# Performance work log

Measured on AMD Instinct MI355X. Metric: run time of the kernel, lower is better.

The kernel has to match this reference:

```python
import jax, jax.numpy as jnp
import numpy as np

N_VARS = 8192
N_CHECKS = 4096
DC = 6          # check degree (edges per check)
DV = 3          # variable degree
N_EDGES = N_CHECKS * DC  # == N_VARS * DV == 24576
NUM_ITERS = 5
BATCH = 2048


def setup_inputs() -> dict:
    key = jax.random.key(0)
    k1, _ = jax.random.split(key)
    channel_llrs = jax.random.normal(k1, (BATCH, N_VARS), dtype=jnp.float32)
    # Regular Tanner graph: edges sorted by check (constant degree DC),
    # variable side is a random permutation with each var appearing DV times.
    H_rows = jnp.asarray(np.repeat(np.arange(N_CHECKS), DC), dtype=jnp.int32)
    rng = np.random.default_rng(0)
    H_cols = jnp.asarray(rng.permutation(np.repeat(np.arange(N_VARS), DV)), dtype=jnp.int32)
    weights = jnp.full((NUM_ITERS, 1), 0.5, dtype=jnp.float32)  # nn.Parameter init
    return {"channel_llrs": channel_llrs, "weights": weights,
            "H_rows": H_rows, "H_cols": H_cols, "n_checks": N_CHECKS}


def _decode(channel_llrs, weights, H_cols, n_checks):
    B, n_vars = channel_llrs.shape
    E = H_cols.shape[0]
    dc = E // n_checks  # constant check degree (edges sorted by check)
    pos = jnp.arange(dc)
    c2v = jnp.zeros((B, E), dtype=channel_llrs.dtype)
    for i in range(weights.shape[0]):
        # variable-node update: sum incoming c2v per variable, exclude self edge
        agg = jnp.zeros((B, n_vars), dtype=channel_llrs.dtype).at[:, H_cols].add(c2v)
        var_llrs = channel_llrs + agg
        v2c = var_llrs[:, H_cols] - c2v                      # [B, E]
        # check-node update (min-sum with self-exclusion), grouped per check
        g = v2c.reshape(B, n_checks, dc)                     # [B, C, dc]
        s = jnp.sign(g)
        prod_s = jnp.prod(s, axis=-1, keepdims=True)
        s_in = jnp.where(s == 0, 1.0, s)                     # torch: sign_in[sign_in==0]=1
        out_sign = prod_s / s_in
        a = jnp.abs(g)
        amin = jnp.min(a, axis=-1, keepdims=True)
        imin = jnp.argmin(a, axis=-1, keepdims=True)
        a2 = jnp.where(pos == imin, jnp.inf, a)
        min2 = jnp.min(a2, axis=-1, keepdims=True)
        min_others = jnp.where(pos == imin, min2, amin)      # min over all-but-self
        c2v = (out_sign * min_others).reshape(B, E) * weights[i]
    final_agg = jnp.zeros((B, n_vars), dtype=channel_llrs.dtype).at[:, H_cols].add(c2v)
    return channel_llrs + final_agg


def reference(channel_llrs, weights, H_rows, H_cols, n_checks):
    # H_rows == repeat(arange(n_checks), dc) by construction; grouping is done
    # via the [n_checks, dc] reshape (same partition as the original per-check loop).
    return _decode(channel_llrs, weights, H_cols, n_checks)
```

## Files before the change

### kernel.cpp

```cpp
#include <hip/hip_runtime.h>
#include <stdint.h>

#define NV    8192
#define NC    4096
#define DC    6
#define DV    3
#define NE    24576
#define NITER 5
#define BATCH 2048


__global__ void build_v2e(const int* __restrict__ cols, int* __restrict__ cnt,
                          unsigned short* __restrict__ v2e_tmp) {
  int e = blockIdx.x * blockDim.x + threadIdx.x;
  if (e >= NE) return;
  int v = cols[e];
  int s = atomicAdd(&cnt[v], 1);
  v2e_tmp[v * DV + s] = (unsigned short)e;
}

__global__ void invert_slots(const unsigned short* __restrict__ v2e_tmp,
                             unsigned short* __restrict__ cslot) {
  int v = blockIdx.x * blockDim.x + threadIdx.x;
  if (v >= NV) return;
  int a = v2e_tmp[v * 3 + 0];
  int b = v2e_tmp[v * 3 + 1];
  int c = v2e_tmp[v * 3 + 2];
  int t;
  if (a > b) { t = a; a = b; b = t; }
  if (b > c) { t = b; b = c; c = t; }
  if (a > b) { t = a; a = b; b = t; }
  cslot[a] = (unsigned short)(0 * NV + v);
  cslot[b] = (unsigned short)(1 * NV + v);
  cslot[c] = (unsigned short)(2 * NV + v);
}


__device__ __forceinline__ int qc(int n) { return (n > 1) ? (n - 1) : 0; }

__global__ __launch_bounds__(64) void greedy_schedule(
    const unsigned short* __restrict__ cslot, unsigned int* __restrict__ slotp) {
  __shared__ unsigned short sl[64][6];
  __shared__ unsigned char perm[64][6];
  __shared__ int qhist[4][32];
  __shared__ int cnt[6][4][32];

  const int l = threadIdx.x;
  const int q = l >> 4;
  const int c = blockIdx.x * 64 + l;

  const unsigned int* cs32 = (const unsigned int*)cslot;
  unsigned int a0 = cs32[c * 3 + 0];
  unsigned int a1 = cs32[c * 3 + 1];
  unsigned int a2 = cs32[c * 3 + 2];
  sl[l][0] = (unsigned short)(a0 & 0xffffu); sl[l][1] = (unsigned short)(a0 >> 16);
  sl[l][2] = (unsigned short)(a1 & 0xffffu); sl[l][3] = (unsigned short)(a1 >> 16);
  sl[l][4] = (unsigned short)(a2 & 0xffffu); sl[l][5] = (unsigned short)(a2 >> 16);

  int bank[6];
#pragma unroll
  for (int k = 0; k < 6; ++k) bank[k] = sl[l][k] & 31;

  for (int t = l; t < 128; t += 64) ((int*)qhist)[t] = 0;
  for (int t = l; t < 768; t += 64) ((int*)cnt)[t] = 0;
  __syncthreads();

#pragma unroll
  for (int k = 0; k < 6; ++k) atomicAdd(&qhist[q][bank[k]], 1);
  __syncthreads();

  int key[6];
#pragma unroll
  for (int k = 0; k < 6; ++k) key[k] = (qhist[q][bank[k]] << 3) | k;
#pragma unroll
  for (int i = 0; i < 5; ++i) {
#pragma unroll
    for (int j2 = 0; j2 < 5 - i; ++j2) {
      if (key[j2] < key[j2 + 1]) {
        int t = key[j2]; key[j2] = key[j2 + 1]; key[j2 + 1] = t;
      }
    }
  }

  unsigned int used = 0;
  for (int j = 0; j < 6; ++j) {
    int placed = -1;
    for (int s = 0; s < 6; ++s) {
      int k = key[s] & 7;
      if (used & (1u << k)) continue;
      int bk = bank[k];
      if (cnt[j][q][bk] == 0) {
        if (atomicAdd(&cnt[j][q][bk], 1) == 0) { placed = k; break; }
        atomicSub(&cnt[j][q][bk], 1);
      }
    }
    if (placed < 0) {
      int bc = 1 << 30;
      for (int k = 0; k < 6; ++k) {
        if (used & (1u << k)) continue;
        int cc = cnt[j][q][bank[k]];
        if (cc < bc) { bc = cc; placed = k; }
      }
      atomicAdd(&cnt[j][q][bank[placed]], 1);
    }
    used |= (1u << placed);
    perm[l][j] = (unsigned char)placed;
    __syncthreads();
  }

  for (int j1 = 0; j1 < 6; ++j1) {
    for (int j2 = j1 + 1; j2 < 6; ++j2) {
      int k1 = perm[l][j1], k2 = perm[l][j2];
      int b1 = bank[k1], b2 = bank[k2];
      if (b1 != b2) {
        int c11 = cnt[j1][q][b1], c12 = cnt[j1][q][b2];
        int c21 = cnt[j2][q][b1], c22 = cnt[j2][q][b2];
        int dOld = qc(c11) + qc(c12) + qc(c21) + qc(c22);
        int dNew = qc(c11 - 1) + qc(c12 + 1) + qc(c21 + 1) + qc(c22 - 1);
        if (dNew < dOld) {
          atomicSub(&cnt[j1][q][b1], 1); atomicAdd(&cnt[j1][q][b2], 1);
          atomicSub(&cnt[j2][q][b2], 1); atomicAdd(&cnt[j2][q][b1], 1);
          perm[l][j1] = (unsigned char)k2; perm[l][j2] = (unsigned char)k1;
        }
      }
      __syncthreads();
    }
  }

  unsigned short pm[6];
#pragma unroll
  for (int j = 0; j < 6; ++j) pm[j] = sl[l][perm[l][j]];
  slotp[0 * NC + c] = (unsigned int)pm[0] | ((unsigned int)pm[1] << 16);
  slotp[1 * NC + c] = (unsigned int)pm[2] | ((unsigned int)pm[3] << 16);
  slotp[2 * NC + c] = (unsigned int)pm[4] | ((unsigned int)pm[5] << 16);
}


__global__ __launch_bounds__(1024, 4) void decode_kernel(
    const float* __restrict__ ch, const float* __restrict__ wts,
    const unsigned int* __restrict__ slotp, float* __restrict__ out) {
  __shared__ float s_msg[NE];
  __shared__ float s_vl[NV];

  const int tid = threadIdx.x;
  const int b = blockIdx.x;
  const float* chrow = ch + (size_t)b * NV;
  const float4* ch4 = (const float4*)chrow;

  float4 chreg[2];
  chreg[0] = ch4[tid];
  chreg[1] = ch4[1024 + tid];

  float w[NITER];
#pragma unroll
  for (int i = 0; i < NITER; ++i) w[i] = wts[i];

  int idx[4][6];
  int vidx[4][6];
#pragma unroll
  for (int r = 0; r < 4; ++r) {
    int c = tid + r * 1024;
    unsigned int p0 = slotp[c];
    unsigned int p1 = slotp[NC + c];
    unsigned int p2 = slotp[2 * NC + c];
    idx[r][0] = (int)(p0 & 0xFFFFu); idx[r][1] = (int)(p0 >> 16);
    idx[r][2] = (int)(p1 & 0xFFFFu); idx[r][3] = (int)(p1 >> 16);
    idx[r][4] = (int)(p2 & 0xFFFFu); idx[r][5] = (int)(p2 >> 16);
#pragma unroll
    for (int j = 0; j < 6; ++j) vidx[r][j] = idx[r][j] & (NV - 1);
  }

  float creg[4][6];
#pragma unroll
  for (int r = 0; r < 4; ++r)
#pragma unroll
    for (int j = 0; j < 6; ++j) creg[r][j] = 0.0f;

  float4* m0 = (float4*)&s_msg[0];
  float4* m1 = (float4*)&s_msg[NV];
  float4* m2 = (float4*)&s_msg[2 * NV];
  float4* vl4 = (float4*)s_vl;

#pragma unroll
  for (int p = 0; p < 2; ++p) vl4[p * 1024 + tid] = chreg[p];
  __syncthreads();

  for (int it = 0; it < NITER; ++it) {
    const float wi = w[it];

    float tv[4][6];
#pragma unroll
    for (int r = 0; r < 4; ++r)
#pragma unroll
      for (int j = 0; j < 6; ++j) tv[r][j] = s_vl[vidx[r][j]];

#pragma unroll
    for (int r = 0; r < 4; ++r) {
      unsigned int u[6];
      float av[6];
      unsigned int xs = 0u;
#pragma unroll
      for (int j = 0; j < 6; ++j) {
        float t = tv[r][j] - creg[r][j];
        unsigned int uu = __float_as_uint(t);
        u[j] = uu;
        xs ^= uu;
        av[j] = __uint_as_float(uu & 0x7FFFFFFFu);
      }
      float m1a = fminf(fminf(av[0], av[1]), av[2]);
      float m1b = fminf(fminf(av[3], av[4]), av[5]);
      float meda = __builtin_amdgcn_fmed3f(av[0], av[1], av[2]);
      float medb = __builtin_amdgcn_fmed3f(av[3], av[4], av[5]);
      float m1v = fminf(m1a, m1b);
      float m2v = fminf(fminf(meda, medb), fmaxf(m1a, m1b));
      const bool anyz = (m1v == 0.0f);
      const float m1w = m1v * wi;
      const float m2w = m2v * wi;
#pragma unroll
      for (int j = 0; j < 6; ++j) {
        float mag = (av[j] == m1v) ? m2w : m1w;
        unsigned int s = (xs ^ u[j]) & 0x80000000u;
        float o = __uint_as_float(__float_as_uint(mag) ^ s);
        if (anyz) o = 0.0f;
        creg[r][j] = o;
        s_msg[idx[r][j]] = o;
      }
    }
    __syncthreads();

    if (it < NITER - 1) {
#pragma unroll
      for (int p = 0; p < 2; ++p) {
        int i4 = p * 1024 + tid;
        float4 c0 = m0[i4], c1 = m1[i4], c2 = m2[i4];
        float4 cr = chreg[p];
        float4 vl;
        vl.x = cr.x + ((c0.x + c1.x) + c2.x);
        vl.y = cr.y + ((c0.y + c1.y) + c2.y);
        vl.z = cr.z + ((c0.z + c1.z) + c2.z);
        vl.w = cr.w + ((c0.w + c1.w) + c2.w);
        vl4[i4] = vl;
      }
      __syncthreads();
    }
  }

  float4* orow4 = (float4*)(out + (size_t)b * NV);
#pragma unroll
  for (int p = 0; p < 2; ++p) {
    int i4 = p * 1024 + tid;
    float4 c0 = m0[i4], c1 = m1[i4], c2 = m2[i4];
    float4 cr = chreg[p];
    float4 o;
    o.x = cr.x + ((c0.x + c1.x) + c2.x);
    o.y = cr.y + ((c0.y + c1.y) + c2.y);
    o.z = cr.z + ((c0.z + c1.z) + c2.z);
    o.w = cr.w + ((c0.w + c1.w) + c2.w);
    orow4[i4] = o;
  }
}


extern "C" void kernel_launch(void* const* d_in, const int* in_sizes, int n_in,
                              void* d_out, int out_size, void* d_ws, size_t ws_size,
                              hipStream_t stream) {
  (void)in_sizes; (void)n_in; (void)out_size; (void)ws_size;

  const float* ch   = (const float*)d_in[0];
  const float* wts  = (const float*)d_in[1];
  const int*  Hcols = (const int*)d_in[3];
  float* out = (float*)d_out;

  char* ws = (char*)d_ws;
  int*            cnt     = (int*)(ws + 0);
  unsigned short* v2e_tmp = (unsigned short*)(ws + 32768);
  unsigned short* cslot   = (unsigned short*)(ws + 81920);
  unsigned int*   slotp   = (unsigned int*)(ws + 131072);

  hipMemsetAsync(cnt, 0, NV * sizeof(int), stream);
  build_v2e<<<(NE + 255) / 256, 256, 0, stream>>>(Hcols, cnt, v2e_tmp);
  invert_slots<<<(NV + 255) / 256, 256, 0, stream>>>(v2e_tmp, cslot);
  greedy_schedule<<<NC / 64, 64, 0, stream>>>(cslot, slotp);

  decode_kernel<<<BATCH, 1024, 0, stream>>>(ch, wts, slotp, out);
}
```

Measured before the change: 138.6 us.

## Schedule check-to-thread assignment per wave to reduce LDS bank conflicts

Replaces the per-check greedy slot permutation with a wave-level scheduler. Each lane picks among its four candidate checks, steered by the remaining bank histogram, and then permutes the chosen check's slots to reduce LDS bank conflicts within each quarter-wave. This reorders which checks each decode thread handles so the scatter and gather to shared memory conflict less. The preprocessing kernel now runs with only 16 blocks and is more serial, which adds setup time.

New measurement: 175.5 us. 1.27x slower.

```diff
diff --git a/kernel.cpp b/kernel.cpp
--- a/kernel.cpp
+++ b/kernel.cpp
@@ -38,101 +38,144 @@
 
 __device__ __forceinline__ int qc(int n) { return (n > 1) ? (n - 1) : 0; }
 
-__global__ __launch_bounds__(64) void greedy_schedule(
+__global__ __launch_bounds__(64) void wave_schedule(
     const unsigned short* __restrict__ cslot, unsigned int* __restrict__ slotp) {
-  __shared__ unsigned short sl[64][6];
-  __shared__ unsigned char perm[64][6];
-  __shared__ int qhist[4][32];
+  __shared__ int grem[4][32];
+  __shared__ int bq[4][32];
   __shared__ int cnt[6][4][32];
 
   const int l = threadIdx.x;
   const int q = l >> 4;
-  const int c = blockIdx.x * 64 + l;
-
+  const int wid = blockIdx.x;
+
+  unsigned short sl[4][6];
+  int bank[4][6];
   const unsigned int* cs32 = (const unsigned int*)cslot;
-  unsigned int a0 = cs32[c * 3 + 0];
-  unsigned int a1 = cs32[c * 3 + 1];
-  unsigned int a2 = cs32[c * 3 + 2];
-  sl[l][0] = (unsigned short)(a0 & 0xffffu); sl[l][1] = (unsigned short)(a0 >> 16);
-  sl[l][2] = (unsigned short)(a1 & 0xffffu); sl[l][3] = (unsigned short)(a1 >> 16);
-  sl[l][4] = (unsigned short)(a2 & 0xffffu); sl[l][5] = (unsigned short)(a2 >> 16);
-
-  int bank[6];
-#pragma unroll
-  for (int k = 0; k < 6; ++k) bank[k] = sl[l][k] & 31;
-
-  for (int t = l; t < 128; t += 64) ((int*)qhist)[t] = 0;
-  for (int t = l; t < 768; t += 64) ((int*)cnt)[t] = 0;
+#pragma unroll
+  for (int r = 0; r < 4; ++r) {
+    int c = r * 1024 + wid * 64 + l;
+    unsigned int a0 = cs32[c * 3 + 0];
+    unsigned int a1 = cs32[c * 3 + 1];
+    unsigned int a2 = cs32[c * 3 + 2];
+    sl[r][0] = (unsigned short)(a0 & 0xffffu); sl[r][1] = (unsigned short)(a0 >> 16);
+    sl[r][2] = (unsigned short)(a1 & 0xffffu); sl[r][3] = (unsigned short)(a1 >> 16);
+    sl[r][4] = (unsigned short)(a2 & 0xffffu); sl[r][5] = (unsigned short)(a2 >> 16);
+#pragma unroll
+    for (int k = 0; k < 6; ++k) bank[r][k] = sl[r][k] & 31;
+  }
+
+  for (int t = l; t < 128; t += 64) ((int*)grem)[t] = 0;
   __syncthreads();
-
-#pragma unroll
-  for (int k = 0; k < 6; ++k) atomicAdd(&qhist[q][bank[k]], 1);
+#pragma unroll
+  for (int r = 0; r < 4; ++r)
+#pragma unroll
+    for (int k = 0; k < 6; ++k) atomicAdd(&grem[q][bank[r][k]], 1);
   __syncthreads();
 
-  int key[6];
-#pragma unroll
-  for (int k = 0; k < 6; ++k) key[k] = (qhist[q][bank[k]] << 3) | k;
-#pragma unroll
-  for (int i = 0; i < 5; ++i) {
-#pragma unroll
-    for (int j2 = 0; j2 < 5 - i; ++j2) {
-      if (key[j2] < key[j2 + 1]) {
-        int t = key[j2]; key[j2] = key[j2 + 1]; key[j2 + 1] = t;
-      }
-    }
-  }
-
-  unsigned int used = 0;
-  for (int j = 0; j < 6; ++j) {
-    int placed = -1;
-    for (int s = 0; s < 6; ++s) {
-      int k = key[s] & 7;
-      if (used & (1u << k)) continue;
-      int bk = bank[k];
-      if (cnt[j][q][bk] == 0) {
-        if (atomicAdd(&cnt[j][q][bk], 1) == 0) { placed = k; break; }
-        atomicSub(&cnt[j][q][bk], 1);
-      }
-    }
-    if (placed < 0) {
-      int bc = 1 << 30;
-      for (int k = 0; k < 6; ++k) {
+  unsigned int taken = 0;
+
+  for (int t = 0; t < 4; ++t) {
+    for (int i = l; i < 128; i += 64) ((int*)bq)[i] = 0;
+    for (int i = l; i < 768; i += 64) ((int*)cnt)[i] = 0;
+    __syncthreads();
+
+    int best = 0, bs = -1;
+#pragma unroll
+    for (int r = 0; r < 4; ++r) {
+      if (taken & (1u << r)) continue;
+      int s = 0;
+#pragma unroll
+      for (int k = 0; k < 6; ++k) s += grem[q][bank[r][k]];
+      if (s > bs) { bs = s; best = r; }
+    }
+    taken |= (1u << best);
+
+    unsigned short msl[6];
+    int mb[6];
+#pragma unroll
+    for (int k = 0; k < 6; ++k) {
+      int vs = sl[0][k];
+      if (best == 1) vs = sl[1][k];
+      if (best == 2) vs = sl[2][k];
+      if (best == 3) vs = sl[3][k];
+      msl[k] = (unsigned short)vs;
+      mb[k] = vs & 31;
+    }
+#pragma unroll
+    for (int k = 0; k < 6; ++k) {
+      atomicSub(&grem[q][mb[k]], 1);
+      atomicAdd(&bq[q][mb[k]], 1);
+    }
+    __syncthreads();
+
+    int key[6];
+#pragma unroll
+    for (int k = 0; k < 6; ++k) key[k] = (bq[q][mb[k]] << 3) | k;
+#pragma unroll
+    for (int i = 0; i < 5; ++i) {
+#pragma unroll
+      for (int j2 = 0; j2 < 5 - i; ++j2) {
+        if (key[j2] < key[j2 + 1]) {
+          int tt = key[j2]; key[j2] = key[j2 + 1]; key[j2 + 1] = tt;
+        }
+      }
+    }
+
+    unsigned char perm[6];
+    unsigned int used = 0;
+    for (int j = 0; j < 6; ++j) {
+      int placed = -1;
+      for (int s = 0; s < 6; ++s) {
+        int k = key[s] & 7;
         if (used & (1u << k)) continue;
-        int cc = cnt[j][q][bank[k]];
-        if (cc < bc) { bc = cc; placed = k; }
-      }
-      atomicAdd(&cnt[j][q][bank[placed]], 1);
-    }
-    used |= (1u << placed);
-    perm[l][j] = (unsigned char)placed;
+        int bk = mb[k];
+        if (cnt[j][q][bk] == 0) {
+          if (atomicAdd(&cnt[j][q][bk], 1) == 0) { placed = k; break; }
+          atomicSub(&cnt[j][q][bk], 1);
+        }
+      }
+      if (placed < 0) {
+        int bc = 1 << 30;
+        for (int k = 0; k < 6; ++k) {
+          if (used & (1u << k)) continue;
+          int cc = cnt[j][q][mb[k]];
+          if (cc < bc) { bc = cc; placed = k; }
+        }
+        atomicAdd(&cnt[j][q][mb[placed]], 1);
+      }
+      used |= (1u << placed);
+      perm[j] = (unsigned char)placed;
+      __syncthreads();
+    }
+
+    for (int j1 = 0; j1 < 6; ++j1) {
+      for (int j2 = j1 + 1; j2 < 6; ++j2) {
+        int k1 = perm[j1], k2 = perm[j2];
+        int b1 = mb[k1], b2 = mb[k2];
+        if (b1 != b2) {
+          int c11 = cnt[j1][q][b1], c12 = cnt[j1][q][b2];
+          int c21 = cnt[j2][q][b1], c22 = cnt[j2][q][b2];
+          int dOld = qc(c11) + qc(c12) + qc(c21) + qc(c22);
+          int dNew = qc(c11 - 1) + qc(c12 + 1) + qc(c21 + 1) + qc(c22 - 1);
+          if (dNew < dOld) {
+            atomicSub(&cnt[j1][q][b1], 1); atomicAdd(&cnt[j1][q][b2], 1);
+            atomicSub(&cnt[j2][q][b2], 1); atomicAdd(&cnt[j2][q][b1], 1);
+            perm[j1] = (unsigned char)k2; perm[j2] = (unsigned char)k1;
+          }
+        }
+        __syncthreads();
+      }
+    }
+
+    unsigned short pm[6];
+#pragma unroll
+    for (int j = 0; j < 6; ++j) pm[j] = msl[perm[j]];
+    int cpos = t * 1024 + wid * 64 + l;
+    slotp[0 * NC + cpos] = (unsigned int)pm[0] | ((unsigned int)pm[1] << 16);
+    slotp[1 * NC + cpos] = (unsigned int)pm[2] | ((unsigned int)pm[3] << 16);
+    slotp[2 * NC + cpos] = (unsigned int)pm[4] | ((unsigned int)pm[5] << 16);
     __syncthreads();
   }
-
-  for (int j1 = 0; j1 < 6; ++j1) {
-    for (int j2 = j1 + 1; j2 < 6; ++j2) {
-      int k1 = perm[l][j1], k2 = perm[l][j2];
-      int b1 = bank[k1], b2 = bank[k2];
-      if (b1 != b2) {
-        int c11 = cnt[j1][q][b1], c12 = cnt[j1][q][b2];
-        int c21 = cnt[j2][q][b1], c22 = cnt[j2][q][b2];
-        int dOld = qc(c11) + qc(c12) + qc(c21) + qc(c22);
-        int dNew = qc(c11 - 1) + qc(c12 + 1) + qc(c21 + 1) + qc(c22 - 1);
-        if (dNew < dOld) {
-          atomicSub(&cnt[j1][q][b1], 1); atomicAdd(&cnt[j1][q][b2], 1);
-          atomicSub(&cnt[j2][q][b2], 1); atomicAdd(&cnt[j2][q][b1], 1);
-          perm[l][j1] = (unsigned char)k2; perm[l][j2] = (unsigned char)k1;
-        }
-      }
-      __syncthreads();
-    }
-  }
-
-  unsigned short pm[6];
-#pragma unroll
-  for (int j = 0; j < 6; ++j) pm[j] = sl[l][perm[l][j]];
-  slotp[0 * NC + c] = (unsigned int)pm[0] | ((unsigned int)pm[1] << 16);
-  slotp[1 * NC + c] = (unsigned int)pm[2] | ((unsigned int)pm[3] << 16);
-  slotp[2 * NC + c] = (unsigned int)pm[4] | ((unsigned int)pm[5] << 16);
 }
 
 
@@ -280,7 +323,7 @@
   hipMemsetAsync(cnt, 0, NV * sizeof(int), stream);
   build_v2e<<<(NE + 255) / 256, 256, 0, stream>>>(Hcols, cnt, v2e_tmp);
   invert_slots<<<(NV + 255) / 256, 256, 0, stream>>>(v2e_tmp, cslot);
-  greedy_schedule<<<NC / 64, 64, 0, stream>>>(cslot, slotp);
+  wave_schedule<<<16, 64, 0, stream>>>(cslot, slotp);
 
   decode_kernel<<<BATCH, 1024, 0, stream>>>(ch, wts, slotp, out);
 }
```

## Replace greedy bank schedule with Kempe-chain edge coloring per quarter-wave

Applied to the files above, without the earlier changes.

The per-check slot permutation is now computed by a bipartite edge-coloring with Kempe-chain swaps instead of a greedy-plus-swap heuristic. Each thread handles the 16 checks that one quarter-wave executes together, and assigns each of a check's 6 edges a distinct step so that LDS bank conflicts in the scatter/gather steps of the decode kernel are minimized. The schedule kernel now runs only 4 blocks of serial per-thread work, so its setup time may grow, while the aim is fewer bank conflicts in the main decode loop.

New measurement: 312.9 us. 2.26x slower.

```diff
diff --git a/kernel.cpp b/kernel.cpp
--- a/kernel.cpp
+++ b/kernel.cpp
@@ -36,103 +36,116 @@
 }
 
 
-__device__ __forceinline__ int qc(int n) { return (n > 1) ? (n - 1) : 0; }
-
-__global__ __launch_bounds__(64) void greedy_schedule(
+__global__ __launch_bounds__(64) void kempe_schedule(
     const unsigned short* __restrict__ cslot, unsigned int* __restrict__ slotp) {
-  __shared__ unsigned short sl[64][6];
-  __shared__ unsigned char perm[64][6];
-  __shared__ int qhist[4][32];
-  __shared__ int cnt[6][4][32];
-
-  const int l = threadIdx.x;
-  const int q = l >> 4;
-  const int c = blockIdx.x * 64 + l;
+  __shared__ unsigned short SL[64][96];
+  __shared__ unsigned char EB[64][96];
+  __shared__ unsigned char LE[64][16][6];
+  __shared__ unsigned char LM[64][16];
+  __shared__ unsigned char BE[64][32][6];
+  __shared__ unsigned char BC[64][32][6];
+  __shared__ unsigned char CH[64][100];
+
+  const int t = threadIdx.x;
+  const int pid = blockIdx.x * 64 + t;
+  const int w = pid >> 4, r = (pid >> 2) & 3, q = pid & 3;
 
   const unsigned int* cs32 = (const unsigned int*)cslot;
-  unsigned int a0 = cs32[c * 3 + 0];
-  unsigned int a1 = cs32[c * 3 + 1];
-  unsigned int a2 = cs32[c * 3 + 2];
-  sl[l][0] = (unsigned short)(a0 & 0xffffu); sl[l][1] = (unsigned short)(a0 >> 16);
-  sl[l][2] = (unsigned short)(a1 & 0xffffu); sl[l][3] = (unsigned short)(a1 >> 16);
-  sl[l][4] = (unsigned short)(a2 & 0xffffu); sl[l][5] = (unsigned short)(a2 >> 16);
-
-  int bank[6];
-#pragma unroll
-  for (int k = 0; k < 6; ++k) bank[k] = sl[l][k] & 31;
-
-  for (int t = l; t < 128; t += 64) ((int*)qhist)[t] = 0;
-  for (int t = l; t < 768; t += 64) ((int*)cnt)[t] = 0;
-  __syncthreads();
-
-#pragma unroll
-  for (int k = 0; k < 6; ++k) atomicAdd(&qhist[q][bank[k]], 1);
-  __syncthreads();
-
-  int key[6];
-#pragma unroll
-  for (int k = 0; k < 6; ++k) key[k] = (qhist[q][bank[k]] << 3) | k;
-#pragma unroll
-  for (int i = 0; i < 5; ++i) {
-#pragma unroll
-    for (int j2 = 0; j2 < 5 - i; ++j2) {
-      if (key[j2] < key[j2 + 1]) {
-        int t = key[j2]; key[j2] = key[j2 + 1]; key[j2 + 1] = t;
-      }
-    }
-  }
-
-  unsigned int used = 0;
-  for (int j = 0; j < 6; ++j) {
-    int placed = -1;
-    for (int s = 0; s < 6; ++s) {
-      int k = key[s] & 7;
-      if (used & (1u << k)) continue;
-      int bk = bank[k];
-      if (cnt[j][q][bk] == 0) {
-        if (atomicAdd(&cnt[j][q][bk], 1) == 0) { placed = k; break; }
-        atomicSub(&cnt[j][q][bk], 1);
-      }
-    }
-    if (placed < 0) {
-      int bc = 1 << 30;
-      for (int k = 0; k < 6; ++k) {
-        if (used & (1u << k)) continue;
-        int cc = cnt[j][q][bank[k]];
-        if (cc < bc) { bc = cc; placed = k; }
-      }
-      atomicAdd(&cnt[j][q][bank[placed]], 1);
-    }
-    used |= (1u << placed);
-    perm[l][j] = (unsigned char)placed;
-    __syncthreads();
-  }
-
-  for (int j1 = 0; j1 < 6; ++j1) {
-    for (int j2 = j1 + 1; j2 < 6; ++j2) {
-      int k1 = perm[l][j1], k2 = perm[l][j2];
-      int b1 = bank[k1], b2 = bank[k2];
-      if (b1 != b2) {
-        int c11 = cnt[j1][q][b1], c12 = cnt[j1][q][b2];
-        int c21 = cnt[j2][q][b1], c22 = cnt[j2][q][b2];
-        int dOld = qc(c11) + qc(c12) + qc(c21) + qc(c22);
-        int dNew = qc(c11 - 1) + qc(c12 + 1) + qc(c21 + 1) + qc(c22 - 1);
-        if (dNew < dOld) {
-          atomicSub(&cnt[j1][q][b1], 1); atomicAdd(&cnt[j1][q][b2], 1);
-          atomicSub(&cnt[j2][q][b2], 1); atomicAdd(&cnt[j2][q][b1], 1);
-          perm[l][j1] = (unsigned char)k2; perm[l][j2] = (unsigned char)k1;
+  for (int i = 0; i < 16; ++i) {
+    int c = r * 1024 + w * 64 + q * 16 + i;
+    unsigned int u0 = cs32[c * 3 + 0];
+    unsigned int u1 = cs32[c * 3 + 1];
+    unsigned int u2 = cs32[c * 3 + 2];
+    unsigned short s0 = (unsigned short)(u0 & 0xffffu), s1 = (unsigned short)(u0 >> 16);
+    unsigned short s2 = (unsigned short)(u1 & 0xffffu), s3 = (unsigned short)(u1 >> 16);
+    unsigned short s4 = (unsigned short)(u2 & 0xffffu), s5 = (unsigned short)(u2 >> 16);
+    SL[t][i * 6 + 0] = s0; SL[t][i * 6 + 1] = s1; SL[t][i * 6 + 2] = s2;
+    SL[t][i * 6 + 3] = s3; SL[t][i * 6 + 4] = s4; SL[t][i * 6 + 5] = s5;
+    EB[t][i * 6 + 0] = s0 & 31; EB[t][i * 6 + 1] = s1 & 31; EB[t][i * 6 + 2] = s2 & 31;
+    EB[t][i * 6 + 3] = s3 & 31; EB[t][i * 6 + 4] = s4 & 31; EB[t][i * 6 + 5] = s5 & 31;
+    LM[t][i] = 0;
+    for (int c2 = 0; c2 < 6; ++c2) LE[t][i][c2] = 0xFF;
+  }
+  for (int b = 0; b < 32; ++b)
+    for (int c2 = 0; c2 < 6; ++c2) { BE[t][b][c2] = 0xFF; BC[t][b][c2] = 0; }
+
+  for (int i = 0; i < 16; ++i) {
+    for (int k = 0; k < 6; ++k) {
+      const int e = i * 6 + k;
+      const int b = EB[t][e];
+      int freeL = (~(int)LM[t][i]) & 0x3F;
+      int c = -1;
+      for (int cc = 0; cc < 6; ++cc)
+        if (((freeL >> cc) & 1) && BC[t][b][cc] == 0) { c = cc; break; }
+      if (c < 0) {
+        int a = __builtin_ctz((unsigned)freeL);
+        int cB = -1;
+        for (int cc = 0; cc < 6; ++cc) if (BC[t][b][cc] == 0) { cB = cc; break; }
+        int done = 0;
+        if (cB >= 0 && BC[t][b][a] == 1) {
+          int n = 0, ok = 1;
+          int cur = BE[t][b][a];
+          while (1) {
+            CH[t][n++] = (unsigned char)cur;
+            int lc = (cur * 171) >> 10;
+            int nxt = LE[t][lc][cB];
+            if (nxt == 0xFF) break;
+            if (n >= 98) { ok = 0; break; }
+            CH[t][n++] = (unsigned char)nxt;
+            int bn = EB[t][nxt];
+            if (BC[t][bn][cB] > 1) { ok = 0; break; }
+            if (BC[t][bn][a] == 0) break;
+            if (BC[t][bn][a] > 1) { ok = 0; break; }
+            if (n >= 98) { ok = 0; break; }
+            cur = BE[t][bn][a];
+          }
+          if (ok) {
+            for (int m = 0; m < n; ++m) {
+              int e2 = CH[t][m]; int f = (m & 1) ? cB : a;
+              int l2 = (e2 * 171) >> 10; int b2 = EB[t][e2];
+              if (LE[t][l2][f] == e2) LE[t][l2][f] = 0xFF;
+              LM[t][l2] &= ~(1 << f);
+              BC[t][b2][f]--;
+              if (BE[t][b2][f] == e2) BE[t][b2][f] = 0xFF;
+            }
+            for (int m = 0; m < n; ++m) {
+              int e2 = CH[t][m]; int tt = (m & 1) ? a : cB;
+              int l2 = (e2 * 171) >> 10; int b2 = EB[t][e2];
+              LE[t][l2][tt] = (unsigned char)e2; LM[t][l2] |= (1 << tt);
+              if (BC[t][b2][tt] == 0) BE[t][b2][tt] = (unsigned char)e2;
+              BC[t][b2][tt]++;
+            }
+            if (LE[t][i][a] == 0xFF) { c = a; done = 1; }
+          }
         }
-      }
-      __syncthreads();
-    }
-  }
-
-  unsigned short pm[6];
-#pragma unroll
-  for (int j = 0; j < 6; ++j) pm[j] = sl[l][perm[l][j]];
-  slotp[0 * NC + c] = (unsigned int)pm[0] | ((unsigned int)pm[1] << 16);
-  slotp[1 * NC + c] = (unsigned int)pm[2] | ((unsigned int)pm[3] << 16);
-  slotp[2 * NC + c] = (unsigned int)pm[4] | ((unsigned int)pm[5] << 16);
+        if (!done && c < 0) {
+          freeL = (~(int)LM[t][i]) & 0x3F;
+          int bcv = 256;
+          for (int cc = 0; cc < 6; ++cc)
+            if ((freeL >> cc) & 1) {
+              int v = BC[t][b][cc];
+              if (v < bcv) { bcv = v; c = cc; }
+            }
+        }
+      }
+      LE[t][i][c] = (unsigned char)e; LM[t][i] |= (1 << c);
+      if (BC[t][b][c] == 0) BE[t][b][c] = (unsigned char)e;
+      BC[t][b][c]++;
+    }
+  }
+
+  for (int i = 0; i < 16; ++i) {
+    unsigned short pm[6];
+    if (LM[t][i] == 0x3F) {
+      for (int c2 = 0; c2 < 6; ++c2) pm[c2] = SL[t][LE[t][i][c2]];
+    } else {
+      for (int c2 = 0; c2 < 6; ++c2) pm[c2] = SL[t][i * 6 + c2];
+    }
+    int cpos = r * 1024 + w * 64 + q * 16 + i;
+    slotp[0 * NC + cpos] = (unsigned int)pm[0] | ((unsigned int)pm[1] << 16);
+    slotp[1 * NC + cpos] = (unsigned int)pm[2] | ((unsigned int)pm[3] << 16);
+    slotp[2 * NC + cpos] = (unsigned int)pm[4] | ((unsigned int)pm[5] << 16);
+  }
 }
 
 
@@ -280,7 +293,7 @@
   hipMemsetAsync(cnt, 0, NV * sizeof(int), stream);
   build_v2e<<<(NE + 255) / 256, 256, 0, stream>>>(Hcols, cnt, v2e_tmp);
   invert_slots<<<(NV + 255) / 256, 256, 0, stream>>>(v2e_tmp, cslot);
-  greedy_schedule<<<NC / 64, 64, 0, stream>>>(cslot, slotp);
+  kempe_schedule<<<4, 64, 0, stream>>>(cslot, slotp);
 
   decode_kernel<<<BATCH, 1024, 0, stream>>>(ch, wts, slotp, out);
 }
```
